# Performance work log

Measured on AMD Instinct MI355X. Metric: run time of the kernel, lower is better.

The kernel has to match this reference:

```python
import jax, jax.numpy as jnp
import numpy as np

B, L, D, H = 2, 2048, 2048, 16
HD = D // H          # head_dim = 128
LD = HD // 4         # latent_dim = 32


def _linear_params(key, fan_in, fan_out):
    kw, kb = jax.random.split(key)
    bound = 1.0 / np.sqrt(fan_in)
    W = jax.random.uniform(kw, (fan_in, fan_out), jnp.float32, -bound, bound)
    b = jax.random.uniform(kb, (fan_out,), jnp.float32, -bound, bound)
    return W, b


def setup_inputs() -> dict:
    key = jax.random.key(0)
    ks = jax.random.split(key, 12)
    x = jax.random.normal(ks[0], (B, L, D), jnp.float32)
    cos = jax.random.uniform(ks[1], (L, HD // 2), jnp.float32)
    sin = jax.random.uniform(ks[2], (L, HD // 2), jnp.float32)
    Wq, bq = _linear_params(ks[3], D, D)
    Wk, bk = _linear_params(ks[4], D, D)
    Wv, bv = _linear_params(ks[5], D, D)
    Wqc, bqc = _linear_params(ks[6], HD, LD)
    Wkc, bkc = _linear_params(ks[7], HD, LD)
    Wvc, bvc = _linear_params(ks[8], HD, LD)
    Wd, bd = _linear_params(ks[9], LD, HD)
    Wo, bo = _linear_params(ks[10], D, D)
    return dict(x=x, cos=cos, sin=sin, Wq=Wq, bq=bq, Wk=Wk, bk=bk, Wv=Wv, bv=bv,
                Wqc=Wqc, bqc=bqc, Wkc=Wkc, bkc=bkc, Wvc=Wvc, bvc=bvc,
                Wd=Wd, bd=bd, Wo=Wo, bo=bo)


def _apply_rope(q, k, cos, sin):
    # q, k: (B, H, L, HD); cos, sin: (L, HD//2) -> broadcast over B, H
    c = cos[None, None, :, :]
    s = sin[None, None, :, :]
    qe, qo = q[..., ::2], q[..., 1::2]
    ke, ko = k[..., ::2], k[..., 1::2]
    q_rot = jnp.stack([qe * c - qo * s, qe * s + qo * c], axis=-1).reshape(q.shape)
    k_rot = jnp.stack([ke * c - ko * s, ke * s + ko * c], axis=-1).reshape(k.shape)
    return q_rot, k_rot


def reference(x, cos, sin, Wq, bq, Wk, bk, Wv, bv,
              Wqc, bqc, Wkc, bkc, Wvc, bvc, Wd, bd, Wo, bo):
    b, l, d = x.shape
    # projections -> (B, H, L, HD)
    q = (x @ Wq + bq).reshape(b, l, H, HD).transpose(0, 2, 1, 3)
    k = (x @ Wk + bk).reshape(b, l, H, HD).transpose(0, 2, 1, 3)
    v = (x @ Wv + bv).reshape(b, l, H, HD).transpose(0, 2, 1, 3)
    q, k = _apply_rope(q, k, cos, sin)
    # low-rank compression into latent_dim
    qc = jnp.einsum('bhld,de->bhle', q, Wqc) + bqc
    kc = jnp.einsum('bhld,de->bhle', k, Wkc) + bkc
    vc = jnp.einsum('bhld,de->bhle', v, Wvc) + bvc
    scores = jnp.einsum('bhqe,bhke->bhqk', qc, kc) / np.sqrt(LD).astype(np.float32)
    causal = jnp.tril(jnp.ones((l, l), dtype=bool))  # True = keep
    scores = jnp.where(causal[None, None], scores, -jnp.inf)
    probs = jax.nn.softmax(scores, axis=-1)
    attn = jnp.einsum('bhqk,bhke->bhqe', probs, vc)
    attn = jnp.einsum('bhle,ed->bhld', attn, Wd) + bd  # decompress to HD
    attn = attn.transpose(0, 2, 1, 3).reshape(b, l, d)
    return attn @ Wo + bo
```

## Files before the change

### kernel.cpp

```cpp
#include <hip/hip_runtime.h>
#include <hip/hip_bf16.h>


#define Bsz 2
#define Lseq 2048
#define Dmod 2048
#define Hn 16
#define HDim 128
#define LDim 32

typedef __bf16 bf16x8 __attribute__((ext_vector_type(8)));
typedef float f32x4 __attribute__((ext_vector_type(4)));
typedef __hip_bfloat16 bf16;

#define GLDS16(g, l)                                                    \
  __builtin_amdgcn_global_load_lds(                                     \
      (const __attribute__((address_space(1))) unsigned int*)(g),       \
      (__attribute__((address_space(3))) unsigned int*)(l), 16, 0, 0)

#define SM_COS 0
#define SM_SIN 131072
#define SM_WC 262144
#define SM_BC 274432
#define SM_WD 274528
#define SM_BD 278624
#define SM_BO 278752
#define SM_BQKV 280800
#define SM_TOT 286944

__global__ void detect_dtype(const ushort* __restrict__ x, int* __restrict__ flag) {
  int t = threadIdx.x;
  int bad = 0;
  for (int k = 0; k < 4; ++k) {
    ushort u = x[t * 4 + k];
    int ex = (u >> 7) & 0xFF;
    if (ex >= 0xC0) bad = 1;
  }
  unsigned long long b = __ballot(bad);
  if (t == 0) *flag = (b != 0ULL) ? 1 : 0;
}

__device__ inline void conv8(const void* src, size_t so, bf16* dst, size_t dof, int f32) {
  if (f32) {
    const float* s = (const float*)src + so;
    bf16 tmp[8] __attribute__((aligned(16)));
    for (int j = 0; j < 8; ++j) tmp[j] = __float2bfloat16(s[j]);
    *(uint4*)&dst[dof] = *(uint4*)tmp;
  } else {
    *(uint4*)&dst[dof] = *(const uint4*)((const ushort*)src + so);
  }
}

__device__ inline float cv1(const void* s, size_t i, int f32) {
  return f32 ? ((const float*)s)[i] : __bfloat162float(((const bf16*)s)[i]);
}

#define NB_T3 3072
#define NB_WV 2048
#define NB_CX 4096
#define NB_PREP 160
#define NB_FBP 256
#define NB_PREP_ALL (NB_T3 + NB_WV + NB_CX + NB_PREP + NB_FBP)

__global__ __launch_bounds__(256) void prep_all(
    const void* xS, const void* cosS, const void* sinS, const void* WqS,
    const void* WkS, const void* WvS, const void* WoS, const void* WqcS,
    const void* WkcS, const void* WvcS, const void* bqcS, const void* bkcS,
    const void* bvcS, const void* WdS, const void* bdS, const void* boS,
    const void* bqS, const void* bkS, const void* bvS,
    bf16* __restrict__ xb, bf16* __restrict__ WvB, bf16* __restrict__ WtQK,
    bf16* __restrict__ WtO, bf16* __restrict__ small, bf16* __restrict__ wctG,
    bf16* __restrict__ wdtG, float* __restrict__ bo_part,
    const int* __restrict__ flagp) {
  __shared__ __align__(16) char shm[16640];
  int f32 = *flagp;
  int blk = blockIdx.x;
  int t = threadIdx.x;

  if (blk < NB_T3) {
    float (*tile)[65] = (float(*)[65])shm;
    int z = blk >> 10, rem = blk & 1023;
    const void* W = (z == 0) ? WqS : (z == 1) ? WkS : WoS;
    bf16* Wt = (z == 2) ? WtO : (WtQK + (size_t)z * 2048 * 2048);
    int n0 = (rem & 31) * 64, k0 = (rem >> 5) * 64;
    int x = (t & 7) * 8, y = t >> 3;
    for (int p = 0; p < 2; ++p) {
      int r = y + p * 32;
      if (f32) {
        const float* src = (const float*)W + (size_t)(k0 + r) * 2048 + n0 + x;
        float4 a = *(const float4*)src;
        float4 b2 = *(const float4*)(src + 4);
        tile[r][x + 0] = a.x; tile[r][x + 1] = a.y; tile[r][x + 2] = a.z; tile[r][x + 3] = a.w;
        tile[r][x + 4] = b2.x; tile[r][x + 5] = b2.y; tile[r][x + 6] = b2.z; tile[r][x + 7] = b2.w;
      } else {
        const ushort* src = (const ushort*)W + (size_t)(k0 + r) * 2048 + n0 + x;
        uint4 u = *(const uint4*)src;
        bf16* e = (bf16*)&u;
        for (int jj = 0; jj < 8; ++jj) tile[r][x + jj] = __bfloat162float(e[jj]);
      }
    }
    __syncthreads();
    for (int p = 0; p < 2; ++p) {
      int n = y + p * 32;
      bf16 tmp[8] __attribute__((aligned(16)));
      for (int jj = 0; jj < 8; ++jj) tmp[jj] = __float2bfloat16(tile[x + jj][n]);
      *(uint4*)&Wt[(size_t)(n0 + n) * 2048 + k0 + x] = *(uint4*)tmp;
    }
  } else if (blk < NB_T3 + NB_WV) {
    size_t e = ((size_t)(blk - NB_T3) * 256 + t) * 8;
    conv8(WvS, e, WvB, e, f32);
  } else if (blk < NB_T3 + NB_WV + NB_CX) {
    size_t e = ((size_t)(blk - NB_T3 - NB_WV) * 256 + t) * 8;
    conv8(xS, e, xb, e, f32);
  } else if (blk < NB_T3 + NB_WV + NB_CX + NB_PREP) {
    int tid = (blk - NB_T3 - NB_WV - NB_CX) * 256 + t;
    if (tid < SM_TOT / 8) {
      size_t e = (size_t)tid * 8;
      const void* src;
      size_t so;
      if (e < SM_SIN) { src = cosS; so = e - SM_COS; }
      else if (e < SM_WC) { src = sinS; so = e - SM_SIN; }
      else if (e < SM_BC) { size_t r = e - SM_WC; src = (r < 4096) ? WqcS : (r < 8192) ? WkcS : WvcS; so = r & 4095; }
      else if (e < SM_WD) { size_t r = e - SM_BC; src = (r < 32) ? bqcS : (r < 64) ? bkcS : bvcS; so = r & 31; }
      else if (e < SM_BD) { src = WdS; so = e - SM_WD; }
      else if (e < SM_BO) { src = bdS; so = e - SM_BD; }
      else if (e < SM_BQKV) { src = boS; so = e - SM_BO; }
      else { size_t r = e - SM_BQKV; src = (r < 2048) ? bqS : (r < 4096) ? bkS : bvS; so = r & 2047; }
      conv8(src, so, small, e, f32);
    } else {
      int idx = tid - SM_TOT / 8;
      for (int i = idx; i < 16384; i += 40960 - SM_TOT / 8) {
        if (i < 12288) {
          int reg = i >> 12, rem2 = i & 4095, n = rem2 >> 7, k = rem2 & 127;
          const void* src = (reg == 0) ? WqcS : (reg == 1) ? WkcS : WvcS;
          wctG[i] = __float2bfloat16(cv1(src, (size_t)k * 32 + n, f32));
        } else {
          int i2 = i - 12288, o = i2 >> 5, e = i2 & 31;
          wdtG[i2] = __float2bfloat16(cv1(WdS, (size_t)e * 128 + o, f32));
        }
      }
    }
  } else {
    float* red = (float*)shm;
    int rem = blk - (NB_T3 + NB_WV + NB_CX + NB_PREP);
    int nb = rem & 15, kb = rem >> 4;
    int col = nb * 128 + (t & 127);
    int half = t >> 7;
    float s = 0.f;
    int kbase = kb * 128 + half * 64;
    for (int i = 0; i < 64; ++i) {
      int k = kbase + i;
      s += cv1(bdS, k & 127, f32) * cv1(WoS, (size_t)k * 2048 + col, f32);
    }
    red[t] = s;
    __syncthreads();
    if (half == 0) bo_part[kb * 2048 + col] = red[t] + red[t + 128];
  }
}

__global__ __launch_bounds__(256) void fold_all(
    const bf16* __restrict__ WvB, const bf16* __restrict__ wctG,
    const bf16* __restrict__ WtO, const bf16* __restrict__ small,
    const void* boS, const float* __restrict__ bo_part, const void* bvS,
    const void* bvcS, const void* WvcS, bf16* __restrict__ Wvt,
    bf16* __restrict__ Wot, float* __restrict__ boF, float* __restrict__ bvF,
    const int* __restrict__ flagp) {
  int blk = blockIdx.x;
  int t = threadIdx.x, lane = t & 63, w = t >> 6;
  int qd = lane >> 4, ln = lane & 15;
  if (blk < 256) {
    int nb = blk & 15, h = blk >> 4;
    f32x4 acc[2][2] = {};
    for (int kt = 0; kt < 4; ++kt) {
      bf16x8 af[2], bfr[2];
      for (int i = 0; i < 2; ++i)
        af[i] = *(const bf16x8*)&wctG[8192 + (i * 16 + ln) * 128 + kt * 32 + qd * 8];
      for (int j = 0; j < 2; ++j)
        bfr[j] = *(const bf16x8*)&WvB[(size_t)(nb * 128 + w * 32 + j * 16 + ln) * 2048 +
                                      h * 128 + kt * 32 + qd * 8];
      for (int i = 0; i < 2; ++i)
        for (int j = 0; j < 2; ++j)
          acc[i][j] = __builtin_amdgcn_mfma_f32_16x16x32_bf16(af[i], bfr[j], acc[i][j], 0, 0, 0);
    }
    for (int i = 0; i < 2; ++i)
      for (int j = 0; j < 2; ++j)
        for (int r = 0; r < 4; ++r) {
          int e = i * 16 + qd * 4 + r;
          int col = nb * 128 + w * 32 + j * 16 + ln;
          Wvt[(size_t)(h * 32 + e) * 2048 + col] = __float2bfloat16(acc[i][j][r]);
        }
  } else if (blk < 512) {
    int rem = blk - 256;
    int mb = rem & 15, h = rem >> 4;
    f32x4 acc[2][2] = {};
    for (int kt = 0; kt < 4; ++kt) {
      bf16x8 af[2], bfr[2];
      for (int i = 0; i < 2; ++i)
        af[i] = *(const bf16x8*)&WtO[(size_t)(mb * 128 + w * 32 + i * 16 + ln) * 2048 +
                                     h * 128 + kt * 32 + qd * 8];
      for (int j = 0; j < 2; ++j)
        bfr[j] = *(const bf16x8*)&small[SM_WD + (j * 16 + ln) * 128 + kt * 32 + qd * 8];
      for (int i = 0; i < 2; ++i)
        for (int j = 0; j < 2; ++j)
          acc[i][j] = __builtin_amdgcn_mfma_f32_16x16x32_bf16(af[i], bfr[j], acc[i][j], 0, 0, 0);
    }
    for (int i = 0; i < 2; ++i)
      for (int j = 0; j < 2; ++j)
        for (int r = 0; r < 4; ++r) {
          int row = mb * 128 + w * 32 + i * 16 + qd * 4 + r;
          int col = h * 32 + j * 16 + ln;
          Wot[(size_t)row * 512 + col] = __float2bfloat16(acc[i][j][r]);
        }
  } else {
    int f32 = *flagp;
    int tid = (blk - 512) * 256 + t;
    if (tid < 2048) {
      float s = cv1(boS, tid, f32);
      for (int kb = 0; kb < 16; ++kb) s += bo_part[kb * 2048 + tid];
      boF[tid] = s;
    } else if (tid < 2560) {
      int j = tid - 2048, h = j >> 5, e = j & 31;
      float s = cv1(bvcS, e, f32);
      for (int hd = 0; hd < 128; ++hd)
        s += cv1(bvS, h * 128 + hd, f32) * cv1(WvcS, (size_t)hd * 32 + e, f32);
      bvF[j] = s;
    }
  }
}

#define ESTR 136
__global__ __launch_bounds__(256) void gemm_qkv(
    const bf16* __restrict__ A, const bf16* __restrict__ Bt,
    const bf16* __restrict__ Wvt, const bf16* __restrict__ small,
    const bf16* __restrict__ wctG, const float* __restrict__ bvF,
    bf16* __restrict__ qc, bf16* __restrict__ kc, bf16* __restrict__ vcT) {
  __shared__ bf16 sh[128 * ESTR];
  const int K = 2048;
  int id = blockIdx.x;
  int t = threadIdx.x;
  int lane = t & 63, w = t >> 6;
  int qd = lane >> 4, ln = lane & 15;

  if (id < 1024) {
    bf16* lA = sh;
    bf16* lB = sh + 4096;
    int bn = id & 31, bm = id >> 5;
    int reg = bn >> 4, h = bn & 15;
    int wm = (w >> 1) * 64, wn = (w & 1) * 64;

    f32x4 acc[4][4] = {};
    const bf16* Ab = A + (size_t)(bm * 128) * K;
    const bf16* Bb = Bt + (size_t)(bn * 128) * K;

    for (int kt = 0; kt < K; kt += 32) {
      for (int p = 0; p < 2; ++p) {
        int slot = t + p * 256;
        int r = slot >> 2, c = (slot & 3) * 8;
        GLDS16(&Ab[(size_t)r * K + kt + c], &lA[slot * 8]);
        GLDS16(&Bb[(size_t)r * K + kt + c], &lB[slot * 8]);
      }
      __syncthreads();
      bf16x8 af[4], bfr[4];
      for (int i = 0; i < 4; ++i) af[i] = *(bf16x8*)&lA[(wm + i * 16 + ln) * 32 + qd * 8];
      for (int j = 0; j < 4; ++j) bfr[j] = *(bf16x8*)&lB[(wn + j * 16 + ln) * 32 + qd * 8];
      for (int i = 0; i < 4; ++i)
        for (int j = 0; j < 4; ++j)
          acc[i][j] = __builtin_amdgcn_mfma_f32_16x16x32_bf16(af[i], bfr[j], acc[i][j], 0, 0, 0);
      __syncthreads();
    }

    for (int j = 0; j < 4; ++j) {
      int col = wn + j * 16 + ln;
      float bv = __bfloat162float(small[SM_BQKV + bn * 128 + col]);
      for (int i = 0; i < 4; ++i)
        for (int r = 0; r < 4; ++r)
          sh[(wm + i * 16 + qd * 4 + r) * ESTR + col] = __float2bfloat16(acc[i][j][r] + bv);
    }
    __syncthreads();

    int r0 = w * 32;
    int b = bm >> 4;
    int bh = b * Hn + h;
    bf16x8 bfr2[2][4];
    for (int nt = 0; nt < 2; ++nt)
      for (int kt = 0; kt < 4; ++kt)
        bfr2[nt][kt] = *(const bf16x8*)&wctG[reg * 4096 + (nt * 16 + ln) * 128 + kt * 32 + qd * 8];
    float bc[2];
    bc[0] = __bfloat162float(small[SM_BC + reg * 32 + ln]);
    bc[1] = __bfloat162float(small[SM_BC + reg * 32 + 16 + ln]);

    for (int mt = 0; mt < 2; ++mt) {
      int lb = r0 + mt * 16 + ln;
      int lg2 = (bm & 15) * 128 + lb;
      f32x4 c2[2] = {};
      for (int kt = 0; kt < 4; ++kt) {
        uint4 u = *(uint4*)&sh[lb * ESTR + kt * 32 + qd * 8];
        bf16* e8 = (bf16*)&u;
        int pbase = kt * 16 + qd * 4;
        uint2 cu = *(const uint2*)&small[SM_COS + (size_t)lg2 * 64 + pbase];
        uint2 su = *(const uint2*)&small[SM_SIN + (size_t)lg2 * 64 + pbase];
        const bf16* cp = (const bf16*)&cu;
        const bf16* sp = (const bf16*)&su;
        for (int j = 0; j < 4; ++j) {
          float cvv = __bfloat162float(cp[j]);
          float svv = __bfloat162float(sp[j]);
          float ev = __bfloat162float(e8[2 * j]);
          float ov = __bfloat162float(e8[2 * j + 1]);
          e8[2 * j] = __float2bfloat16(ev * cvv - ov * svv);
          e8[2 * j + 1] = __float2bfloat16(ev * svv + ov * cvv);
        }
        bf16x8 a = *(bf16x8*)&u;
        c2[0] = __builtin_amdgcn_mfma_f32_16x16x32_bf16(a, bfr2[0][kt], c2[0], 0, 0, 0);
        c2[1] = __builtin_amdgcn_mfma_f32_16x16x32_bf16(a, bfr2[1][kt], c2[1], 0, 0, 0);
      }
      int lgbase = (bm & 15) * 128 + r0 + mt * 16 + qd * 4;
      bf16* dst = (reg == 0) ? qc : kc;
      for (int nt = 0; nt < 2; ++nt)
        for (int r = 0; r < 4; ++r)
          dst[((size_t)bh * Lseq + lgbase + r) * 32 + nt * 16 + ln] =
              __float2bfloat16(c2[nt][r] + bc[nt]);
    }
  } else {
    bf16* lA = sh;
    bf16* lB = sh + 2048;
    int rem = id - 1024;
    int nb = rem & 7, bm = rem >> 3;
    int wm = (w >> 1) * 32, wn = (w & 1) * 32;

    f32x4 acc[2][2] = {};
    const bf16* Ab = A + (size_t)(bm * 64) * K;
    const bf16* Bb = Wvt + (size_t)(nb * 64) * K;

    int r = t >> 2, c = (t & 3) * 8;
    for (int kt = 0; kt < K; kt += 32) {
      GLDS16(&Ab[(size_t)r * K + kt + c], &lA[t * 8]);
      GLDS16(&Bb[(size_t)r * K + kt + c], &lB[t * 8]);
      __syncthreads();
      bf16x8 af[2], bfr[2];
      for (int i = 0; i < 2; ++i) af[i] = *(bf16x8*)&lA[(wm + i * 16 + ln) * 32 + qd * 8];
      for (int j = 0; j < 2; ++j) bfr[j] = *(bf16x8*)&lB[(wn + j * 16 + ln) * 32 + qd * 8];
      for (int i = 0; i < 2; ++i)
        for (int j = 0; j < 2; ++j)
          acc[i][j] = __builtin_amdgcn_mfma_f32_16x16x32_bf16(af[i], bfr[j], acc[i][j], 0, 0, 0);
      __syncthreads();
    }

    int b = bm >> 5;
    for (int j = 0; j < 2; ++j) {
      int n = nb * 64 + wn + j * 16 + ln;
      float bb = bvF[n];
      for (int i = 0; i < 2; ++i) {
        int lloc = (bm & 31) * 64 + wm + i * 16 + qd * 4;
        bf16 p4[4] __attribute__((aligned(8)));
        for (int rr = 0; rr < 4; ++rr) p4[rr] = __float2bfloat16(acc[i][j][rr] + bb);
        *(uint2*)&vcT[((size_t)(b * 512 + n)) * 2048 + lloc] = *(uint2*)p4;
      }
    }
  }
}

__global__ __launch_bounds__(256) void gemm_bias_out(const bf16* __restrict__ A,
                                                     const bf16* __restrict__ Bt,
                                                     const float* __restrict__ bias,
                                                     void* __restrict__ C,
                                                     int M, int N, int K,
                                                     const int* __restrict__ flagp) {
  __shared__ bf16 lA[128 * 32];
  __shared__ bf16 lB[128 * 32];
  int f32out = *flagp;
  int bm = blockIdx.y, bn = blockIdx.x;
  int t = threadIdx.x;
  int lane = t & 63, w = t >> 6;
  int wm = (w >> 1) * 64, wn = (w & 1) * 64;
  int qd = lane >> 4, ln = lane & 15;

  f32x4 acc[4][4] = {};
  const bf16* Ab = A + (size_t)(bm * 128) * K;
  const bf16* Bb = Bt + (size_t)(bn * 128) * K;

  for (int kt = 0; kt < K; kt += 32) {
    for (int p = 0; p < 2; ++p) {
      int slot = t + p * 256;
      int r = slot >> 2, c = (slot & 3) * 8;
      GLDS16(&Ab[(size_t)r * K + kt + c], &lA[slot * 8]);
      GLDS16(&Bb[(size_t)r * K + kt + c], &lB[slot * 8]);
    }
    __syncthreads();
    bf16x8 af[4], bfr[4];
    for (int i = 0; i < 4; ++i) af[i] = *(bf16x8*)&lA[(wm + i * 16 + ln) * 32 + qd * 8];
    for (int j = 0; j < 4; ++j) bfr[j] = *(bf16x8*)&lB[(wn + j * 16 + ln) * 32 + qd * 8];
    for (int i = 0; i < 4; ++i)
      for (int j = 0; j < 4; ++j)
        acc[i][j] = __builtin_amdgcn_mfma_f32_16x16x32_bf16(af[i], bfr[j], acc[i][j], 0, 0, 0);
    __syncthreads();
  }
  for (int i = 0; i < 4; ++i)
    for (int j = 0; j < 4; ++j) {
      int col = bn * 128 + wn + j * 16 + ln;
      float bv = bias[col];
      for (int r = 0; r < 4; ++r) {
        int row = bm * 128 + wm + i * 16 + qd * 4 + r;
        float v = acc[i][j][r] + bv;
        if (f32out) ((float*)C)[(size_t)row * N + col] = v;
        else ((bf16*)C)[(size_t)row * N + col] = __float2bfloat16(v);
      }
    }
}

__global__ __launch_bounds__(256) void flash32(const bf16* __restrict__ qc,
                                               const bf16* __restrict__ kc,
                                               const bf16* __restrict__ vcT,
                                               bf16* __restrict__ attn) {
  __shared__ bf16 pbuf[4][16 * 72];
  __shared__ float oL[4][16][33];
  __shared__ float mL[4][16];
  __shared__ float lsL[4][16];
  int t = threadIdx.x;
  int lane = t & 63, w = t >> 6;
  int qd = lane >> 4, ln = lane & 15;
  int blk = blockIdx.x;
  int j = blk & 127;
  int bh = blk >> 7, h = bh & 15, b = bh >> 4;
  int q0 = j * 16;

  bf16x8 qf = *(const bf16x8*)&qc[((size_t)bh * Lseq + q0 + ln) * 32 + qd * 8];

  f32x4 o0 = {}, o1 = {};
  float m[4], ls[4];
  for (int r = 0; r < 4; ++r) { m[r] = -1e30f; ls[r] = 0.f; }
  const float scale2 = 0.17677669529663687f * 1.4426950408889634f;

  int n64 = (q0 + 16 + 63) >> 6;
  int nw = (n64 + 3) >> 2;
  int c0 = w * nw;
  int c1 = min(c0 + nw, n64);

  bf16* pb = pbuf[w];
  bf16x8 kf[4];
  if (c0 < c1) {
    int k0 = c0 * 64;
    for (int c = 0; c < 4; ++c)
      kf[c] = *(const bf16x8*)&kc[((size_t)bh * Lseq + k0 + c * 16 + ln) * 32 + qd * 8];
  }
  for (int ci = c0; ci < c1; ++ci) {
    int k0 = ci * 64;
    f32x4 s[4];
    for (int c = 0; c < 4; ++c) {
      f32x4 z = {};
      s[c] = __builtin_amdgcn_mfma_f32_16x16x32_bf16(qf, kf[c], z, 0, 0, 0);
    }
    size_t vbase = ((size_t)bh * 32 + ln) * Lseq + k0 + qd * 8;
    bf16x8 vf00 = *(const bf16x8*)&vcT[vbase];
    bf16x8 vf01 = *(const bf16x8*)&vcT[vbase + 32];
    bf16x8 vf10 = *(const bf16x8*)&vcT[vbase + (size_t)16 * Lseq];
    bf16x8 vf11 = *(const bf16x8*)&vcT[vbase + (size_t)16 * Lseq + 32];
    if (ci + 1 < c1) {
      int k0n = k0 + 64;
      for (int c = 0; c < 4; ++c)
        kf[c] = *(const bf16x8*)&kc[((size_t)bh * Lseq + k0n + c * 16 + ln) * 32 + qd * 8];
    }
    float sv[4][4], alpha[4];
    for (int r = 0; r < 4; ++r) {
      int qrow = q0 + qd * 4 + r;
      for (int c = 0; c < 4; ++c)
        sv[c][r] = (k0 + c * 16 + ln <= qrow) ? s[c][r] * scale2 : -1e30f;
    }
    for (int r = 0; r < 4; ++r) {
      float mx = fmaxf(fmaxf(sv[0][r], sv[1][r]), fmaxf(sv[2][r], sv[3][r]));
      for (int off = 1; off < 16; off <<= 1) mx = fmaxf(mx, __shfl_xor(mx, off, 64));
      float mn = fmaxf(m[r], mx);
      alpha[r] = exp2f(m[r] - mn);
      m[r] = mn;
      float rs = 0.f;
      for (int c = 0; c < 4; ++c) { sv[c][r] = exp2f(sv[c][r] - mn); rs += sv[c][r]; }
      ls[r] = ls[r] * alpha[r] + rs;
      o0[r] *= alpha[r];
      o1[r] *= alpha[r];
    }
    for (int r = 0; r < 4; ++r)
      for (int c = 0; c < 4; ++c)
        pb[(qd * 4 + r) * 72 + c * 16 + ln] = __float2bfloat16(sv[c][r]);
    asm volatile("s_waitcnt lgkmcnt(0)" ::: "memory");
    bf16x8 pf0 = *(bf16x8*)&pb[ln * 72 + qd * 8];
    bf16x8 pf1 = *(bf16x8*)&pb[ln * 72 + 32 + qd * 8];
    o0 = __builtin_amdgcn_mfma_f32_16x16x32_bf16(pf0, vf00, o0, 0, 0, 0);
    o0 = __builtin_amdgcn_mfma_f32_16x16x32_bf16(pf1, vf01, o0, 0, 0, 0);
    o1 = __builtin_amdgcn_mfma_f32_16x16x32_bf16(pf0, vf10, o1, 0, 0, 0);
    o1 = __builtin_amdgcn_mfma_f32_16x16x32_bf16(pf1, vf11, o1, 0, 0, 0);
  }

  for (int r = 0; r < 4; ++r)
    for (int off = 1; off < 16; off <<= 1) ls[r] += __shfl_xor(ls[r], off, 64);

  for (int r = 0; r < 4; ++r) {
    int row = qd * 4 + r;
    oL[w][row][ln] = o0[r];
    oL[w][row][16 + ln] = o1[r];
    if (ln == 0) { mL[w][row] = m[r]; lsL[w][row] = ls[r]; }
  }
  __syncthreads();

  for (int idx = t; idx < 512; idx += 256) {
    int row = idx >> 5, col = idx & 31;
    float m0 = mL[0][row], m1 = mL[1][row], m2 = mL[2][row], m3 = mL[3][row];
    float ms = fmaxf(fmaxf(m0, m1), fmaxf(m2, m3));
    float e0 = exp2f(m0 - ms), e1 = exp2f(m1 - ms);
    float e2 = exp2f(m2 - ms), e3 = exp2f(m3 - ms);
    float lsum = lsL[0][row] * e0 + lsL[1][row] * e1 + lsL[2][row] * e2 + lsL[3][row] * e3;
    float val = oL[0][row][col] * e0 + oL[1][row][col] * e1 +
                oL[2][row][col] * e2 + oL[3][row][col] * e3;
    int l = q0 + row;
    attn[((size_t)(b * Lseq + l)) * 512 + h * 32 + col] = __float2bfloat16(val / lsum);
  }
}

extern "C" void kernel_launch(void* const* d_in, const int* in_sizes, int n_in,
                              void* d_out, int out_size, void* d_ws, size_t ws_size,
                              hipStream_t stream) {
  const void* x = d_in[0];
  const void* cosS = d_in[1];
  const void* sinS = d_in[2];
  const void* Wq = d_in[3];
  const void* bq = d_in[4];
  const void* Wk = d_in[5];
  const void* bk = d_in[6];
  const void* Wv = d_in[7];
  const void* bv = d_in[8];
  const void* Wqc = d_in[9];
  const void* bqc = d_in[10];
  const void* Wkc = d_in[11];
  const void* bkc = d_in[12];
  const void* Wvc = d_in[13];
  const void* bvc = d_in[14];
  const void* Wd = d_in[15];
  const void* bd = d_in[16];
  const void* Wo = d_in[17];
  const void* bo = d_in[18];

  char* ws = (char*)d_ws;
  size_t off = 0;
  auto alloc = [&](size_t bytes) {
    char* p = ws + off;
    off += (bytes + 255) & ~(size_t)255;
    return p;
  };
  int* flag = (int*)alloc(256);
  bf16* small = (bf16*)alloc((size_t)SM_TOT * 2);
  bf16* wctG = (bf16*)alloc((size_t)12288 * 2);
  bf16* wdtG = (bf16*)alloc((size_t)4096 * 2);
  bf16* xb = (bf16*)alloc((size_t)4096 * 2048 * 2);
  bf16* WvB = (bf16*)alloc((size_t)2048 * 2048 * 2);
  bf16* WtQK = (bf16*)alloc((size_t)4096 * 2048 * 2);
  bf16* WtO = (bf16*)alloc((size_t)2048 * 2048 * 2);
  bf16* Wvt = (bf16*)alloc((size_t)512 * 2048 * 2);
  bf16* Wot = (bf16*)alloc((size_t)2048 * 512 * 2);
  float* bo_part = (float*)alloc((size_t)16 * 2048 * 4);
  float* boF = (float*)alloc((size_t)2048 * 4);
  float* bvF = (float*)alloc((size_t)512 * 4);
  bf16* qcW = (bf16*)alloc((size_t)65536 * 32 * 2);
  bf16* kcW = (bf16*)alloc((size_t)65536 * 32 * 2);
  bf16* vcTW = (bf16*)alloc((size_t)65536 * 32 * 2);
  bf16* attnW = (bf16*)alloc((size_t)4096 * 512 * 2);

  dim3 tb(256);
  detect_dtype<<<1, 64, 0, stream>>>((const ushort*)x, flag);
  prep_all<<<NB_PREP_ALL, tb, 0, stream>>>(
      x, cosS, sinS, Wq, Wk, Wv, Wo, Wqc, Wkc, Wvc, bqc, bkc, bvc, Wd, bd, bo,
      bq, bk, bv, xb, WvB, WtQK, WtO, small, wctG, wdtG, bo_part, flag);
  fold_all<<<522, tb, 0, stream>>>(WvB, wctG, WtO, small, bo, bo_part, bv, bvc,
                                   Wvc, Wvt, Wot, boF, bvF, flag);
  gemm_qkv<<<1536, tb, 0, stream>>>(xb, WtQK, Wvt, small, wctG, bvF, qcW, kcW, vcTW);
  flash32<<<4096, tb, 0, stream>>>(qcW, kcW, vcTW, attnW);
  gemm_bias_out<<<dim3(16, 32), tb, 0, stream>>>(attnW, Wot, boF, d_out, 4096, 2048,
                                                 512, flag);
}
```

Before: 394.2 us.

## Fuse dtype detection into prep kernel, reorder blocks, lazy softmax rescale

Result: faster. 381.0 us (-3.4%).

```diff
diff --git a/kernel.cpp b/kernel.cpp
--- a/kernel.cpp
+++ b/kernel.cpp
@@ -28,18 +28,6 @@
 #define SM_BQKV 280800
 #define SM_TOT 286944
 
-__global__ void detect_dtype(const ushort* __restrict__ x, int* __restrict__ flag) {
-  int t = threadIdx.x;
-  int bad = 0;
-  for (int k = 0; k < 4; ++k) {
-    ushort u = x[t * 4 + k];
-    int ex = (u >> 7) & 0xFF;
-    if (ex >= 0xC0) bad = 1;
-  }
-  unsigned long long b = __ballot(bad);
-  if (t == 0) *flag = (b != 0ULL) ? 1 : 0;
-}
-
 __device__ inline void conv8(const void* src, size_t so, bf16* dst, size_t dof, int f32) {
   if (f32) {
     const float* s = (const float*)src + so;
@@ -55,12 +43,12 @@
   return f32 ? ((const float*)s)[i] : __bfloat162float(((const bf16*)s)[i]);
 }
 
-#define NB_T3 3072
-#define NB_WV 2048
-#define NB_CX 4096
-#define NB_PREP 160
-#define NB_FBP 256
-#define NB_PREP_ALL (NB_T3 + NB_WV + NB_CX + NB_PREP + NB_FBP)
+#define PB_FBP 0
+#define PB_T3 256
+#define PB_WV 3328
+#define PB_CX 5376
+#define PB_SM 9472
+#define NB_PREP_ALL 9632
 
 __global__ __launch_bounds__(256) void prep_all(
     const void* xS, const void* cosS, const void* sinS, const void* WqS,
@@ -70,16 +58,44 @@
     const void* bqS, const void* bkS, const void* bvS,
     bf16* __restrict__ xb, bf16* __restrict__ WvB, bf16* __restrict__ WtQK,
     bf16* __restrict__ WtO, bf16* __restrict__ small, bf16* __restrict__ wctG,
-    bf16* __restrict__ wdtG, float* __restrict__ bo_part,
-    const int* __restrict__ flagp) {
+    float* __restrict__ bo_part, int* __restrict__ flagW) {
   __shared__ __align__(16) char shm[16640];
-  int f32 = *flagp;
+  __shared__ int sflag;
   int blk = blockIdx.x;
   int t = threadIdx.x;
 
-  if (blk < NB_T3) {
+  if (t < 64) {
+    int bad = 0;
+    for (int k = 0; k < 4; ++k) {
+      ushort u = ((const ushort*)xS)[t * 4 + k];
+      int ex = (u >> 7) & 0xFF;
+      if (ex >= 0xC0) bad = 1;
+    }
+    unsigned long long bl = __ballot(bad);
+    if (t == 0) sflag = (bl != 0ULL) ? 1 : 0;
+  }
+  __syncthreads();
+  int f32 = sflag;
+  if (blk == 0 && t == 0) *flagW = f32;
+
+  if (blk < PB_T3) {
+    float* red = (float*)shm;
+    int nb = blk & 15, kb = blk >> 4;
+    int col = nb * 128 + (t & 127);
+    int half = t >> 7;
+    float s = 0.f;
+    int kbase = kb * 128 + half * 64;
+    for (int i = 0; i < 64; ++i) {
+      int k = kbase + i;
+      s += cv1(bdS, k & 127, f32) * cv1(WoS, (size_t)k * 2048 + col, f32);
+    }
+    red[t] = s;
+    __syncthreads();
+    if (half == 0) bo_part[kb * 2048 + col] = red[t] + red[t + 128];
+  } else if (blk < PB_WV) {
     float (*tile)[65] = (float(*)[65])shm;
-    int z = blk >> 10, rem = blk & 1023;
+    int rem0 = blk - PB_T3;
+    int z = rem0 >> 10, rem = rem0 & 1023;
     const void* W = (z == 0) ? WqS : (z == 1) ? WkS : WoS;
     bf16* Wt = (z == 2) ? WtO : (WtQK + (size_t)z * 2048 * 2048);
     int n0 = (rem & 31) * 64, k0 = (rem >> 5) * 64;
@@ -106,14 +122,14 @@
       for (int jj = 0; jj < 8; ++jj) tmp[jj] = __float2bfloat16(tile[x + jj][n]);
       *(uint4*)&Wt[(size_t)(n0 + n) * 2048 + k0 + x] = *(uint4*)tmp;
     }
-  } else if (blk < NB_T3 + NB_WV) {
-    size_t e = ((size_t)(blk - NB_T3) * 256 + t) * 8;
+  } else if (blk < PB_CX) {
+    size_t e = ((size_t)(blk - PB_WV) * 256 + t) * 8;
     conv8(WvS, e, WvB, e, f32);
-  } else if (blk < NB_T3 + NB_WV + NB_CX) {
-    size_t e = ((size_t)(blk - NB_T3 - NB_WV) * 256 + t) * 8;
+  } else if (blk < PB_SM) {
+    size_t e = ((size_t)(blk - PB_CX) * 256 + t) * 8;
     conv8(xS, e, xb, e, f32);
-  } else if (blk < NB_T3 + NB_WV + NB_CX + NB_PREP) {
-    int tid = (blk - NB_T3 - NB_WV - NB_CX) * 256 + t;
+  } else {
+    int tid = (blk - PB_SM) * 256 + t;
     if (tid < SM_TOT / 8) {
       size_t e = (size_t)tid * 8;
       const void* src;
@@ -129,32 +145,12 @@
       conv8(src, so, small, e, f32);
     } else {
       int idx = tid - SM_TOT / 8;
-      for (int i = idx; i < 16384; i += 40960 - SM_TOT / 8) {
-        if (i < 12288) {
-          int reg = i >> 12, rem2 = i & 4095, n = rem2 >> 7, k = rem2 & 127;
-          const void* src = (reg == 0) ? WqcS : (reg == 1) ? WkcS : WvcS;
-          wctG[i] = __float2bfloat16(cv1(src, (size_t)k * 32 + n, f32));
-        } else {
-          int i2 = i - 12288, o = i2 >> 5, e = i2 & 31;
-          wdtG[i2] = __float2bfloat16(cv1(WdS, (size_t)e * 128 + o, f32));
-        }
-      }
-    }
-  } else {
-    float* red = (float*)shm;
-    int rem = blk - (NB_T3 + NB_WV + NB_CX + NB_PREP);
-    int nb = rem & 15, kb = rem >> 4;
-    int col = nb * 128 + (t & 127);
-    int half = t >> 7;
-    float s = 0.f;
-    int kbase = kb * 128 + half * 64;
-    for (int i = 0; i < 64; ++i) {
-      int k = kbase + i;
-      s += cv1(bdS, k & 127, f32) * cv1(WoS, (size_t)k * 2048 + col, f32);
-    }
-    red[t] = s;
-    __syncthreads();
-    if (half == 0) bo_part[kb * 2048 + col] = red[t] + red[t + 128];
+      for (int i = idx; i < 12288; i += 40960 - SM_TOT / 8) {
+        int reg = i >> 12, rem2 = i & 4095, n = rem2 >> 7, k = rem2 & 127;
+        const void* src = (reg == 0) ? WqcS : (reg == 1) ? WkcS : WvcS;
+        wctG[i] = __float2bfloat16(cv1(src, (size_t)k * 32 + n, f32));
+      }
+    }
   }
 }
 
@@ -459,7 +455,7 @@
       for (int c = 0; c < 4; ++c)
         kf[c] = *(const bf16x8*)&kc[((size_t)bh * Lseq + k0n + c * 16 + ln) * 32 + qd * 8];
     }
-    float sv[4][4], alpha[4];
+    float sv[4][4];
     for (int r = 0; r < 4; ++r) {
       int qrow = q0 + qd * 4 + r;
       for (int c = 0; c < 4; ++c)
@@ -468,14 +464,17 @@
     for (int r = 0; r < 4; ++r) {
       float mx = fmaxf(fmaxf(sv[0][r], sv[1][r]), fmaxf(sv[2][r], sv[3][r]));
       for (int off = 1; off < 16; off <<= 1) mx = fmaxf(mx, __shfl_xor(mx, off, 64));
-      float mn = fmaxf(m[r], mx);
-      alpha[r] = exp2f(m[r] - mn);
-      m[r] = mn;
+      if (!__all(mx <= m[r] + 8.f)) {
+        float mn = fmaxf(m[r], mx);
+        float alpha = exp2f(m[r] - mn);
+        m[r] = mn;
+        ls[r] *= alpha;
+        o0[r] *= alpha;
+        o1[r] *= alpha;
+      }
       float rs = 0.f;
-      for (int c = 0; c < 4; ++c) { sv[c][r] = exp2f(sv[c][r] - mn); rs += sv[c][r]; }
-      ls[r] = ls[r] * alpha[r] + rs;
-      o0[r] *= alpha[r];
-      o1[r] *= alpha[r];
+      for (int c = 0; c < 4; ++c) { sv[c][r] = exp2f(sv[c][r] - m[r]); rs += sv[c][r]; }
+      ls[r] += rs;
     }
     for (int r = 0; r < 4; ++r)
       for (int c = 0; c < 4; ++c)
@@ -547,7 +546,6 @@
   int* flag = (int*)alloc(256);
   bf16* small = (bf16*)alloc((size_t)SM_TOT * 2);
   bf16* wctG = (bf16*)alloc((size_t)12288 * 2);
-  bf16* wdtG = (bf16*)alloc((size_t)4096 * 2);
   bf16* xb = (bf16*)alloc((size_t)4096 * 2048 * 2);
   bf16* WvB = (bf16*)alloc((size_t)2048 * 2048 * 2);
   bf16* WtQK = (bf16*)alloc((size_t)4096 * 2048 * 2);
@@ -563,10 +561,9 @@
   bf16* attnW = (bf16*)alloc((size_t)4096 * 512 * 2);
 
   dim3 tb(256);
-  detect_dtype<<<1, 64, 0, stream>>>((const ushort*)x, flag);
   prep_all<<<NB_PREP_ALL, tb, 0, stream>>>(
       x, cosS, sinS, Wq, Wk, Wv, Wo, Wqc, Wkc, Wvc, bqc, bkc, bvc, Wd, bd, bo,
-      bq, bk, bv, xb, WvB, WtQK, WtO, small, wctG, wdtG, bo_part, flag);
+      bq, bk, bv, xb, WvB, WtQK, WtO, small, wctG, bo_part, flag);
   fold_all<<<522, tb, 0, stream>>>(WvB, wctG, WtO, small, bo, bo_part, bv, bvc,
                                    Wvc, Wvt, Wot, boF, bvF, flag);
   gemm_qkv<<<1536, tb, 0, stream>>>(xb, WtQK, Wvt, small, wctG, bvF, qcW, kcW, vcTW);
```
